# Performance work log

Hardware: AMD Instinct MI355X
Metric: run time of the kernel (lower is better)

## Reference

```python
import jax, jax.numpy as jnp
import numpy as np

D_MODEL = 512
TOP_K = 4


def setup_inputs() -> dict:
    key = jax.random.key(0)
    ks = jax.random.split(key, 7)
    B, L, D = 16, 2048, D_MODEL
    s = 1.0 / np.sqrt(D)
    return {
        "x": jax.random.normal(ks[0], (B, L, D), dtype=jnp.float32),
        "Wq": jax.random.uniform(ks[1], (D, D), jnp.float32, -s, s),
        "bq": jax.random.uniform(ks[2], (D,), jnp.float32, -s, s),
        "Wk": jax.random.uniform(ks[3], (D, D), jnp.float32, -s, s),
        "bk": jax.random.uniform(ks[4], (D,), jnp.float32, -s, s),
        "Wv": jax.random.uniform(ks[5], (D, D), jnp.float32, -s, s),
        "bv": jax.random.uniform(ks[6], (D,), jnp.float32, -s, s),
    }


def reference(x, Wq, bq, Wk, bk, Wv, bv):
    B, L, D = x.shape
    # Linear projections (torch Linear: x @ W.T + b)
    Q = jnp.einsum('bld,ed->ble', x, Wq) + bq
    K = jnp.einsum('bld,ed->ble', x, Wk) + bk
    V = jnp.einsum('bld,ed->ble', x, Wv) + bv
    # FFT autocorrelation along time axis
    q_fft = jnp.fft.rfft(Q, axis=1)
    k_fft = jnp.fft.rfft(K, axis=1)
    corr = jnp.fft.irfft(q_fft * jnp.conj(k_fft), n=L, axis=1)  # [B, L, D]
    mean_corr = corr.mean(axis=-1)                               # [B, L]
    topk_vals, topk_idx = jax.lax.top_k(mean_corr, TOP_K)        # [B, K]
    weights = jax.nn.softmax(topk_vals, axis=-1)                 # [B, K]
    # torch.roll(V[b], shifts=lag, dims=0): out[t] = V[b, (t - lag) % L]
    t = jnp.arange(L)
    gather_idx = (t[None, None, :] - topk_idx[:, :, None]) % L   # [B, K, L]
    rolled = V[jnp.arange(B)[:, None, None], gather_idx]         # [B, K, L, D]
    agg = jnp.einsum('bk,bkld->bld', weights, rolled)
    return agg
```

## Files before the change

kernel.cpp:

```cpp
#include <hip/hip_runtime.h>
#include <math.h>

typedef unsigned short u16;
typedef unsigned int   u32;
typedef __attribute__((ext_vector_type(8))) __bf16 bf16x8;
typedef __attribute__((ext_vector_type(4))) float  f32x4;

#define BB 16
#define LL 2048
#define DD 512
#define NF 1025
#define TOPK 4

static const size_t OFF_XB  = 0;
static const size_t OFF_XTB = OFF_XB  + 8388608;
static const size_t OFF_GT  = OFF_XTB + 8388608;
static const size_t OFF_XC  = OFF_GT  + 16777216;
static const size_t OFF_BBM = OFF_XC  + 8388608;
static const size_t OFF_S   = OFF_BBM + 262144;
static const size_t OFF_W   = OFF_S   + (size_t)BB * NF * 2;
static const size_t OFF_I   = OFF_W   + BB * TOPK;

__device__ __forceinline__ u16 f2bf(float f) {
    u32 u = __float_as_uint(f);
    return (u16)((u + 0x7fffu + ((u >> 16) & 1u)) >> 16);
}
__device__ __forceinline__ float bf2f(u16 h) {
    return __uint_as_float(((u32)h) << 16);
}
__device__ __forceinline__ void gload16(const void* g, void* l) {
    __builtin_amdgcn_global_load_lds((const __attribute__((address_space(1))) void*)g,
                                     (__attribute__((address_space(3))) void*)l, 16, 0, 0);
}
__device__ __forceinline__ float2 cmul(float2 u, float2 v) {
    return make_float2(u.x * v.x - u.y * v.y, u.x * v.y + u.y * v.x);
}
__device__ __forceinline__ float2 cadd(float2 u, float2 v) { return make_float2(u.x + v.x, u.y + v.y); }
__device__ __forceinline__ float2 csub(float2 u, float2 v) { return make_float2(u.x - v.x, u.y - v.y); }

template<int M, int SGN>
__device__ __forceinline__ void radix4(const float2* __restrict__ src,
                                       float2* __restrict__ dst,
                                       const float2* __restrict__ twl, int tid) {
#pragma unroll
    for (int r = 0; r < 2; r++) {
        int w = tid + 256 * r;
        int k = w & (M - 1);
        int jm = w - k;
        float2 a = src[w], b = src[w + 512], c = src[w + 1024], d = src[w + 1536];
        float2 t0 = cadd(a, c), t1 = csub(a, c), t2 = cadd(b, d), bd = csub(b, d);
        float2 t3 = (SGN > 0) ? make_float2(bd.y, -bd.x)
                              : make_float2(-bd.y, bd.x);
        float2 T1 = twl[jm];
        float2 T2 = twl[2 * jm];
        float2 T3 = cmul(T1, T2);
        int o = 4 * jm + k;
        dst[o]         = cadd(t0, t2);
        dst[o + M]     = cmul(cadd(t1, t3), T1);
        dst[o + 2 * M] = cmul(csub(t0, t2), T2);
        dst[o + 3 * M] = cmul(csub(t1, t3), T3);
    }
}

template<int SGN>
__device__ __forceinline__ void fft2048(float2* __restrict__ A, float2* __restrict__ Bf,
                                        const float2* __restrict__ twl, int tid) {
#pragma unroll
    for (int r = 0; r < 4; r++) {
        int j = tid + 256 * r;
        float2 a = A[j], b = A[j + 1024];
        Bf[2 * j]     = cadd(a, b);
        Bf[2 * j + 1] = cmul(csub(a, b), twl[j]);
    }
    __syncthreads();
    radix4<2,   SGN>(Bf, A, twl, tid); __syncthreads();
    radix4<8,   SGN>(A, Bf, twl, tid); __syncthreads();
    radix4<32,  SGN>(Bf, A, twl, tid); __syncthreads();
    radix4<128, SGN>(A, Bf, twl, tid); __syncthreads();
    radix4<512, SGN>(Bf, A, twl, tid); __syncthreads();
}

__global__ __launch_bounds__(256) void k_transpose(const float* __restrict__ in,
                                                   u16* __restrict__ xb,
                                                   u16* __restrict__ xtb) {
    __shared__ u16 tile[32][33];
    int tx = threadIdx.x & 31, ty = threadIdx.x >> 5;
    int d0 = blockIdx.x * 32, t0 = blockIdx.y * 32, b = blockIdx.z;
    const float* ip = in + (size_t)b * LL * DD;
    u16* xbp = xb + (size_t)b * LL * DD;
    u16* xtp = xtb + (size_t)b * DD * LL;
#pragma unroll
    for (int i = 0; i < 4; i++) {
        float v = ip[(size_t)(t0 + ty + 8 * i) * DD + d0 + tx];
        u16 h = f2bf(v);
        xbp[(size_t)(t0 + ty + 8 * i) * DD + d0 + tx] = h;
        tile[ty + 8 * i][tx] = h;
    }
    __syncthreads();
#pragma unroll
    for (int i = 0; i < 4; i++)
        xtp[(size_t)(d0 + ty + 8 * i) * LL + t0 + tx] = tile[tx][ty + 8 * i];
}

__global__ __launch_bounds__(256) void k_gemm1(const float* __restrict__ Wq,
                                               const float* __restrict__ Wk,
                                               u16* __restrict__ Bm) {
    __shared__ float As[16][68];
    __shared__ float Bs[16][68];
    int t = threadIdx.x;
    int tx = t & 15, ty = t >> 4;
    int m0 = blockIdx.x * 64, n0 = blockIdx.y * 64;
    float acc[4][4] = {};
    for (int k0 = 0; k0 < DD; k0 += 16) {
#pragma unroll
        for (int r = 0; r < 4; r++) {
            As[ty][tx + 16 * r] = Wq[(size_t)(k0 + ty) * DD + m0 + tx + 16 * r];
            Bs[ty][tx + 16 * r] = Wk[(size_t)(k0 + ty) * DD + n0 + tx + 16 * r];
        }
        __syncthreads();
#pragma unroll
        for (int k = 0; k < 16; k++) {
            float4 a4 = *(const float4*)&As[k][ty * 4];
            float4 b4 = *(const float4*)&Bs[k][tx * 4];
            float a[4] = {a4.x, a4.y, a4.z, a4.w};
            float b[4] = {b4.x, b4.y, b4.z, b4.w};
#pragma unroll
            for (int i = 0; i < 4; i++)
#pragma unroll
                for (int j = 0; j < 4; j++) acc[i][j] += a[i] * b[j];
        }
        __syncthreads();
    }
#pragma unroll
    for (int i = 0; i < 4; i++) {
        uint2 o;
        o.x = (u32)f2bf(acc[i][0]) | ((u32)f2bf(acc[i][1]) << 16);
        o.y = (u32)f2bf(acc[i][2]) | ((u32)f2bf(acc[i][3]) << 16);
        *(uint2*)&Bm[(size_t)(m0 + ty * 4 + i) * DD + n0 + tx * 4] = o;
    }
}

__global__ __launch_bounds__(256) void k_castwv(const float* __restrict__ Wv,
                                                u16* __restrict__ Bm) {
    int i = blockIdx.x * 256 + threadIdx.x;
    Bm[DD * DD + i] = f2bf(Wv[i]);
}

__global__ __launch_bounds__(256, 2) void k_gemm2(const u16* __restrict__ Ab,
                                                  const u16* __restrict__ Bm,
                                                  float* __restrict__ GT) {
    __shared__ u16 smem[16384];
    u16* As = smem;
    u16* Bs = smem + 8192;
    int t = threadIdx.x;
    int wave = t >> 6, lane = t & 63;
    int l15 = lane & 15, l4 = lane >> 4;
    int qr = wave & 1, qc = wave >> 1;
    int m0 = blockIdx.x * 128, n0 = blockIdx.y * 128;

    f32x4 acc[4][4];
#pragma unroll
    for (int i = 0; i < 4; i++)
#pragma unroll
        for (int j = 0; j < 4; j++) acc[i][j] = (f32x4){0.f, 0.f, 0.f, 0.f};

    const u16* Ag = Ab + (size_t)m0 * DD;
    const u16* Bg = Bm + (size_t)n0 * DD;
    int a_base = (qr * 64 + l15) * 64 + l4 * 8;
    int b_base = (qc * 64 + l15) * 64 + l4 * 8;

    for (int k0 = 0; k0 < DD; k0 += 64) {
#pragma unroll
        for (int n = 0; n < 4; n++) {
            int c = wave * 256 + n * 64 + lane;
            int row = c >> 3, col = (c & 7) * 8;
            gload16(Ag + (size_t)row * DD + k0 + col, (char*)As + (size_t)(wave * 256 + n * 64) * 16);
            gload16(Bg + (size_t)row * DD + k0 + col, (char*)Bs + (size_t)(wave * 256 + n * 64) * 16);
        }
        __syncthreads();
#pragma unroll
        for (int kk = 0; kk < 64; kk += 32) {
            bf16x8 af[4], bq[4];
#pragma unroll
            for (int i = 0; i < 4; i++) af[i] = *(const bf16x8*)(As + a_base + i * 1024 + kk);
#pragma unroll
            for (int j = 0; j < 4; j++) bq[j] = *(const bf16x8*)(Bs + b_base + j * 1024 + kk);
#pragma unroll
            for (int i = 0; i < 4; i++)
#pragma unroll
                for (int j = 0; j < 4; j++)
                    acc[i][j] = __builtin_amdgcn_mfma_f32_16x16x32_bf16(af[i], bq[j], acc[i][j], 0, 0, 0);
        }
        __syncthreads();
    }

    float4* tb4 = (float4*)smem;
    int bidx = m0 >> 11;
    int tbase = m0 & 2047;
#pragma unroll
    for (int p = 0; p < 2; p++) {
        __syncthreads();
        if (qc == p) {
#pragma unroll
            for (int j = 0; j < 4; j++) {
                int nloc = j * 16 + l15;
#pragma unroll
                for (int i = 0; i < 4; i++) {
                    int tq = qr * 16 + i * 4 + l4;
                    tb4[nloc * 32 + (tq ^ (nloc & 31))] = *(float4*)&acc[i][j];
                }
            }
        }
        __syncthreads();
#pragma unroll
        for (int u = 0; u < 8; u++) {
            int idx4 = u * 256 + t;
            int nloc = idx4 >> 5, c4 = idx4 & 31;
            float4 v = tb4[nloc * 32 + (c4 ^ (nloc & 31))];
            *(float4*)&GT[((size_t)bidx * DD + n0 + p * 64 + nloc) * LL + tbase + c4 * 4] = v;
        }
    }
}

__global__ __launch_bounds__(256, 2) void k_gemm3(const u16* __restrict__ Ab,
                                                  const u16* __restrict__ Bm,
                                                  const float* __restrict__ bv,
                                                  float* __restrict__ out) {
    __shared__ u16 smem[16384];
    u16* As = smem;
    u16* Bs = smem + 8192;
    int t = threadIdx.x;
    int wave = t >> 6, lane = t & 63;
    int l15 = lane & 15, l4 = lane >> 4;
    int qr = wave & 1, qc = wave >> 1;
    int m0 = blockIdx.x * 128, n0 = blockIdx.y * 128;

    f32x4 acc[4][4];
#pragma unroll
    for (int i = 0; i < 4; i++)
#pragma unroll
        for (int j = 0; j < 4; j++) acc[i][j] = (f32x4){0.f, 0.f, 0.f, 0.f};

    const u16* Ag = Ab + (size_t)m0 * DD;
    const u16* Bg = Bm + (size_t)DD * DD + (size_t)n0 * DD;
    int a_base = (qr * 64 + l15) * 64 + l4 * 8;
    int b_base = (qc * 64 + l15) * 64 + l4 * 8;

    for (int k0 = 0; k0 < DD; k0 += 64) {
#pragma unroll
        for (int n = 0; n < 4; n++) {
            int c = wave * 256 + n * 64 + lane;
            int row = c >> 3, col = (c & 7) * 8;
            gload16(Ag + (size_t)row * DD + k0 + col, (char*)As + (size_t)(wave * 256 + n * 64) * 16);
            gload16(Bg + (size_t)row * DD + k0 + col, (char*)Bs + (size_t)(wave * 256 + n * 64) * 16);
        }
        __syncthreads();
#pragma unroll
        for (int kk = 0; kk < 64; kk += 32) {
            bf16x8 af[4], bq[4];
#pragma unroll
            for (int i = 0; i < 4; i++) af[i] = *(const bf16x8*)(As + a_base + i * 1024 + kk);
#pragma unroll
            for (int j = 0; j < 4; j++) bq[j] = *(const bf16x8*)(Bs + b_base + j * 1024 + kk);
#pragma unroll
            for (int i = 0; i < 4; i++)
#pragma unroll
                for (int j = 0; j < 4; j++)
                    acc[i][j] = __builtin_amdgcn_mfma_f32_16x16x32_bf16(af[i], bq[j], acc[i][j], 0, 0, 0);
        }
        __syncthreads();
    }

    float*  tb  = (float*)smem;
    float4* tb4 = (float4*)smem;
#pragma unroll
    for (int p = 0; p < 2; p++) {
        __syncthreads();
        if (qr == p) {
#pragma unroll
            for (int j = 0; j < 4; j++) {
                int nloc = qc * 64 + j * 16 + l15;
#pragma unroll
                for (int i = 0; i < 4; i++) {
#pragma unroll
                    for (int r = 0; r < 4; r++) {
                        int mloc = i * 16 + l4 * 4 + r;
                        int nc = ((nloc >> 2) ^ (mloc & 31)) << 2;
                        tb[mloc * 128 + nc + (nloc & 3)] = acc[i][j][r];
                    }
                }
            }
        }
        __syncthreads();
#pragma unroll
        for (int u = 0; u < 8; u++) {
            int idx4 = u * 256 + t;
            int mloc = idx4 >> 5, c4 = idx4 & 31;
            float4 v = tb4[mloc * 32 + (c4 ^ (mloc & 31))];
            float4 bias = *(const float4*)&bv[n0 + c4 * 4];
            v.x += bias.x; v.y += bias.y; v.z += bias.z; v.w += bias.w;
            *(float4*)&out[(size_t)(m0 + p * 64 + mloc) * DD + n0 + c4 * 4] = v;
        }
    }
}

__global__ void k_zero(float* __restrict__ S) {
    int i = blockIdx.x * 256 + threadIdx.x;
    int n = BB * NF * 2;
    for (; i < n; i += gridDim.x * 256) S[i] = 0.f;
}

__global__ __launch_bounds__(256) void k_fft(const u16* __restrict__ XTB,
                                             const float* __restrict__ GT,
                                             float* __restrict__ S) {
    __shared__ float2 A[2048];
    __shared__ float2 Bf[2048];
    __shared__ float2 twl[1024];
    __shared__ float2 Sacc[NF];
    int tid = threadIdx.x;
    int grp = blockIdx.x;
    int b = blockIdx.y;
    for (int j = tid; j < 1024; j += 256) {
        float sn, cs;
        sincosf(-6.283185307179586f * (float)j / 2048.0f, &sn, &cs);
        twl[j] = make_float2(cs, sn);
    }
    for (int f = tid; f < NF; f += 256) Sacc[f] = make_float2(0.f, 0.f);
    for (int c = 0; c < 8; c++) {
        int d = grp * 8 + c;
        const u16*   xp = XTB + ((size_t)b * DD + d) * LL;
        const float* gp = GT  + ((size_t)b * DD + d) * LL;
        __syncthreads();
#pragma unroll
        for (int r = 0; r < 8; r++) {
            int i = tid + 256 * r;
            A[i] = make_float2(bf2f(xp[i]), gp[i]);
        }
        __syncthreads();
        fft2048<1>(A, Bf, twl, tid);
        for (int f = tid; f <= 1024; f += 256) {
            float2 p = A[f];
            float2 q = A[(2048 - f) & 2047];
            float ar = 0.5f * (p.x + q.x), ai = 0.5f * (p.y - q.y);
            float dr = p.x - q.x, di = p.y + q.y;
            float gr = 0.5f * di, gi = -0.5f * dr;
            Sacc[f].x += ar * gr + ai * gi;
            Sacc[f].y += ai * gr - ar * gi;
        }
    }
    __syncthreads();
    float* Sg = S + (size_t)b * NF * 2;
    for (int f = tid; f < NF; f += 256) {
        atomicAdd(&Sg[2 * f], Sacc[f].x);
        atomicAdd(&Sg[2 * f + 1], Sacc[f].y);
    }
}

__global__ __launch_bounds__(256) void k_topk(const float* __restrict__ S,
                                              float* __restrict__ wts,
                                              int* __restrict__ idxs) {
    __shared__ float2 A[2048];
    __shared__ float2 Bf[2048];
    __shared__ float2 twl[1024];
    __shared__ float cv[2048];
    __shared__ float rv[256];
    __shared__ int ri[256];
    __shared__ float topv[TOPK];
    __shared__ int topi[TOPK];
    int tid = threadIdx.x;
    int b = blockIdx.x;
    const float* Sg = S + (size_t)b * NF * 2;
    for (int j = tid; j < 1024; j += 256) {
        float sn, cs;
        sincosf(6.283185307179586f * (float)j / 2048.0f, &sn, &cs);
        twl[j] = make_float2(cs, sn);
    }
    for (int f = tid; f < 2048; f += 256) {
        float re, im;
        if (f <= 1024) { re = Sg[2 * f]; im = Sg[2 * f + 1]; }
        else { re = Sg[2 * (2048 - f)]; im = -Sg[2 * (2048 - f) + 1]; }
        A[f] = make_float2(re, im);
    }
    __syncthreads();
    fft2048<-1>(A, Bf, twl, tid);
    const float scale = 1.0f / ((float)LL * (float)DD);
    for (int f = tid; f < 2048; f += 256) cv[f] = A[f].x * scale;
    __syncthreads();
    for (int r = 0; r < TOPK; r++) {
        float best = -3.0e38f;
        int bi = 0x7fffffff;
        for (int f = tid; f < 2048; f += 256) {
            bool taken = false;
            for (int q = 0; q < r; q++) taken |= (topi[q] == f);
            float v = cv[f];
            if (!taken && (v > best || (v == best && f < bi))) { best = v; bi = f; }
        }
        rv[tid] = best; ri[tid] = bi;
        __syncthreads();
        for (int s = 128; s > 0; s >>= 1) {
            if (tid < s) {
                float v2 = rv[tid + s]; int i2 = ri[tid + s];
                if (v2 > rv[tid] || (v2 == rv[tid] && i2 < ri[tid])) { rv[tid] = v2; ri[tid] = i2; }
            }
            __syncthreads();
        }
        if (tid == 0) { topv[r] = rv[0]; topi[r] = ri[0]; }
        __syncthreads();
    }
    if (tid == 0) {
        float mx = topv[0];
        float e[TOPK], sum = 0.f;
        for (int k = 0; k < TOPK; k++) { e[k] = expf(topv[k] - mx); sum += e[k]; }
        for (int k = 0; k < TOPK; k++) {
            wts[b * TOPK + k] = e[k] / sum;
            idxs[b * TOPK + k] = topi[k];
        }
    }
}

__global__ __launch_bounds__(128) void k_combine(const u16* __restrict__ XB,
                                                 const float* __restrict__ wts,
                                                 const int* __restrict__ idxs,
                                                 u16* __restrict__ XC) {
    int l = blockIdx.x, b = blockIdx.y;
    int t = threadIdx.x;
    const ushort4* Xb = (const ushort4*)(XB + (size_t)b * LL * DD);
    float4 acc = make_float4(0.f, 0.f, 0.f, 0.f);
#pragma unroll
    for (int k = 0; k < TOPK; k++) {
        float w = wts[b * TOPK + k];
        int r = (l - idxs[b * TOPK + k]) & (LL - 1);
        ushort4 v = Xb[(size_t)r * 128 + t];
        acc.x += w * bf2f(v.x); acc.y += w * bf2f(v.y);
        acc.z += w * bf2f(v.z); acc.w += w * bf2f(v.w);
    }
    ushort4 o;
    o.x = f2bf(acc.x); o.y = f2bf(acc.y); o.z = f2bf(acc.z); o.w = f2bf(acc.w);
    ((ushort4*)(XC + (size_t)b * LL * DD))[(size_t)l * 128 + t] = o;
}

extern "C" void kernel_launch(void* const* d_in, const int* in_sizes, int n_in,
                              void* d_out, int out_size, void* d_ws, size_t ws_size,
                              hipStream_t stream) {
    const float* x  = (const float*)d_in[0];
    const float* Wq = (const float*)d_in[1];
    const float* Wk = (const float*)d_in[3];
    const float* Wv = (const float*)d_in[5];
    const float* bv = (const float*)d_in[6];
    (void)in_sizes; (void)n_in; (void)out_size; (void)ws_size;

    float* ws  = (float*)d_ws;
    u16*   XB  = (u16*)(ws + OFF_XB);
    u16*   XTB = (u16*)(ws + OFF_XTB);
    float* GT  = ws + OFF_GT;
    u16*   XC  = (u16*)(ws + OFF_XC);
    u16*   BM  = (u16*)(ws + OFF_BBM);
    float* S   = ws + OFF_S;
    float* wts = ws + OFF_W;
    int*   idx = (int*)(ws + OFF_I);
    float* out = (float*)d_out;

    k_transpose<<<dim3(DD / 32, LL / 32, BB), 256, 0, stream>>>(x, XB, XTB);
    k_gemm1<<<dim3(DD / 64, DD / 64), 256, 0, stream>>>(Wq, Wk, BM);
    k_castwv<<<1024, 256, 0, stream>>>(Wv, BM);
    k_gemm2<<<dim3((BB * LL) / 128, DD / 128), 256, 0, stream>>>(XB, BM, GT);
    k_zero<<<32, 256, 0, stream>>>(S);
    k_fft<<<dim3(64, BB), 256, 0, stream>>>(XTB, GT, S);
    k_topk<<<BB, 256, 0, stream>>>(S, wts, idx);
    k_combine<<<dim3(LL, BB), 128, 0, stream>>>(XB, wts, idx, XC);
    k_gemm3<<<dim3((BB * LL) / 128, DD / 128), 256, 0, stream>>>(XC, BM, bv, out);
}
```

Measured before the change: 347.1 us.

## Fuse preprocessing kernels, store GT in bf16, and streamline FFT staging

Merges transpose, Wq·Wk GEMM, Wv cast and S zeroing into one launch with block-range dispatch, cutting launch count. The gemm2 output GT is stored as bf16, halving its write and the FFT's read traffic at some precision cost. The FFT kernel fuses the first radix-2 stage into the load, keeps spectrum accumulators in registers instead of LDS, and computes T2 as T1 squared instead of a second twiddle lookup. radix4 also gains redundant duplicate stores that are later overwritten, adding extra LDS writes.

Result: faster. 326.8 us (-5.9%).

```diff
diff --git a/kernel.cpp b/kernel.cpp
--- a/kernel.cpp
+++ b/kernel.cpp
@@ -14,8 +14,8 @@
 
 static const size_t OFF_XB  = 0;
 static const size_t OFF_XTB = OFF_XB  + 8388608;
-static const size_t OFF_GT  = OFF_XTB + 8388608;
-static const size_t OFF_XC  = OFF_GT  + 16777216;
+static const size_t OFF_GTB = OFF_XTB + 8388608;
+static const size_t OFF_XC  = OFF_GTB + 8388608;
 static const size_t OFF_BBM = OFF_XC  + 8388608;
 static const size_t OFF_S   = OFF_BBM + 262144;
 static const size_t OFF_W   = OFF_S   + (size_t)BB * NF * 2;
@@ -52,103 +52,107 @@
         float2 t3 = (SGN > 0) ? make_float2(bd.y, -bd.x)
                               : make_float2(-bd.y, bd.x);
         float2 T1 = twl[jm];
-        float2 T2 = twl[2 * jm];
+        float2 T2 = cmul(T1, T1);
         float2 T3 = cmul(T1, T2);
         int o = 4 * jm + k;
         dst[o]         = cadd(t0, t2);
         dst[o + M]     = cmul(cadd(t1, t3), T1);
+        dst[o + 2 * M] = cmul(csub(t1, t3), T3);
+        dst[o + M]     = cmul(cadd(t1, t3), T1);
         dst[o + 2 * M] = cmul(csub(t0, t2), T2);
         dst[o + 3 * M] = cmul(csub(t1, t3), T3);
     }
 }
 
 template<int SGN>
-__device__ __forceinline__ void fft2048(float2* __restrict__ A, float2* __restrict__ Bf,
-                                        const float2* __restrict__ twl, int tid) {
-#pragma unroll
-    for (int r = 0; r < 4; r++) {
-        int j = tid + 256 * r;
-        float2 a = A[j], b = A[j + 1024];
-        Bf[2 * j]     = cadd(a, b);
-        Bf[2 * j + 1] = cmul(csub(a, b), twl[j]);
-    }
-    __syncthreads();
-    radix4<2,   SGN>(Bf, A, twl, tid); __syncthreads();
-    radix4<8,   SGN>(A, Bf, twl, tid); __syncthreads();
-    radix4<32,  SGN>(Bf, A, twl, tid); __syncthreads();
-    radix4<128, SGN>(A, Bf, twl, tid); __syncthreads();
-    radix4<512, SGN>(Bf, A, twl, tid); __syncthreads();
-}
-
-__global__ __launch_bounds__(256) void k_transpose(const float* __restrict__ in,
-                                                   u16* __restrict__ xb,
-                                                   u16* __restrict__ xtb) {
-    __shared__ u16 tile[32][33];
-    int tx = threadIdx.x & 31, ty = threadIdx.x >> 5;
-    int d0 = blockIdx.x * 32, t0 = blockIdx.y * 32, b = blockIdx.z;
-    const float* ip = in + (size_t)b * LL * DD;
-    u16* xbp = xb + (size_t)b * LL * DD;
-    u16* xtp = xtb + (size_t)b * DD * LL;
-#pragma unroll
-    for (int i = 0; i < 4; i++) {
-        float v = ip[(size_t)(t0 + ty + 8 * i) * DD + d0 + tx];
-        u16 h = f2bf(v);
-        xbp[(size_t)(t0 + ty + 8 * i) * DD + d0 + tx] = h;
-        tile[ty + 8 * i][tx] = h;
-    }
-    __syncthreads();
-#pragma unroll
-    for (int i = 0; i < 4; i++)
-        xtp[(size_t)(d0 + ty + 8 * i) * LL + t0 + tx] = tile[tx][ty + 8 * i];
-}
-
-__global__ __launch_bounds__(256) void k_gemm1(const float* __restrict__ Wq,
-                                               const float* __restrict__ Wk,
-                                               u16* __restrict__ Bm) {
-    __shared__ float As[16][68];
-    __shared__ float Bs[16][68];
-    int t = threadIdx.x;
-    int tx = t & 15, ty = t >> 4;
-    int m0 = blockIdx.x * 64, n0 = blockIdx.y * 64;
-    float acc[4][4] = {};
-    for (int k0 = 0; k0 < DD; k0 += 16) {
-#pragma unroll
-        for (int r = 0; r < 4; r++) {
-            As[ty][tx + 16 * r] = Wq[(size_t)(k0 + ty) * DD + m0 + tx + 16 * r];
-            Bs[ty][tx + 16 * r] = Wk[(size_t)(k0 + ty) * DD + n0 + tx + 16 * r];
-        }
-        __syncthreads();
-#pragma unroll
-        for (int k = 0; k < 16; k++) {
-            float4 a4 = *(const float4*)&As[k][ty * 4];
-            float4 b4 = *(const float4*)&Bs[k][tx * 4];
-            float a[4] = {a4.x, a4.y, a4.z, a4.w};
-            float b[4] = {b4.x, b4.y, b4.z, b4.w};
-#pragma unroll
-            for (int i = 0; i < 4; i++)
-#pragma unroll
-                for (int j = 0; j < 4; j++) acc[i][j] += a[i] * b[j];
-        }
-        __syncthreads();
-    }
-#pragma unroll
-    for (int i = 0; i < 4; i++) {
-        uint2 o;
-        o.x = (u32)f2bf(acc[i][0]) | ((u32)f2bf(acc[i][1]) << 16);
-        o.y = (u32)f2bf(acc[i][2]) | ((u32)f2bf(acc[i][3]) << 16);
-        *(uint2*)&Bm[(size_t)(m0 + ty * 4 + i) * DD + n0 + tx * 4] = o;
-    }
-}
-
-__global__ __launch_bounds__(256) void k_castwv(const float* __restrict__ Wv,
-                                                u16* __restrict__ Bm) {
-    int i = blockIdx.x * 256 + threadIdx.x;
-    Bm[DD * DD + i] = f2bf(Wv[i]);
+__device__ __forceinline__ void fft_r4_chain(float2* __restrict__ b1, float2* __restrict__ b2,
+                                             const float2* __restrict__ twl, int tid) {
+    radix4<2,   SGN>(b1, b2, twl, tid); __syncthreads();
+    radix4<8,   SGN>(b2, b1, twl, tid); __syncthreads();
+    radix4<32,  SGN>(b1, b2, twl, tid); __syncthreads();
+    radix4<128, SGN>(b2, b1, twl, tid); __syncthreads();
+    radix4<512, SGN>(b1, b2, twl, tid); __syncthreads();
+}
+
+__global__ __launch_bounds__(256) void k_pre(const float* __restrict__ x,
+                                             const float* __restrict__ Wq,
+                                             const float* __restrict__ Wk,
+                                             const float* __restrict__ Wv,
+                                             u16* __restrict__ xb,
+                                             u16* __restrict__ xtb,
+                                             u16* __restrict__ Bm,
+                                             float* __restrict__ S) {
+    __shared__ char sh[8704];
+    int bid = blockIdx.x;
+    int tid = threadIdx.x;
+    if (bid < 16384) {
+        u16 (*tile)[33] = (u16(*)[33])sh;
+        int bx = bid & 15, by = (bid >> 4) & 63, bz = bid >> 10;
+        int tx = tid & 31, ty = tid >> 5;
+        int d0 = bx * 32, t0 = by * 32;
+        const float* ip = x + (size_t)bz * LL * DD;
+        u16* xbp = xb + (size_t)bz * LL * DD;
+        u16* xtp = xtb + (size_t)bz * DD * LL;
+#pragma unroll
+        for (int i = 0; i < 4; i++) {
+            float v = ip[(size_t)(t0 + ty + 8 * i) * DD + d0 + tx];
+            u16 h = f2bf(v);
+            xbp[(size_t)(t0 + ty + 8 * i) * DD + d0 + tx] = h;
+            tile[ty + 8 * i][tx] = h;
+        }
+        __syncthreads();
+#pragma unroll
+        for (int i = 0; i < 4; i++)
+            xtp[(size_t)(d0 + ty + 8 * i) * LL + t0 + tx] = tile[tx][ty + 8 * i];
+    } else if (bid < 16448) {
+        int g = bid - 16384;
+        float (*As)[68] = (float(*)[68])sh;
+        float (*Bs)[68] = (float(*)[68])(sh + 4352);
+        int tx = tid & 15, ty = tid >> 4;
+        int m0 = (g & 7) * 64, n0 = (g >> 3) * 64;
+        float acc[4][4] = {};
+        for (int k0 = 0; k0 < DD; k0 += 16) {
+#pragma unroll
+            for (int r = 0; r < 4; r++) {
+                As[ty][tx + 16 * r] = Wq[(size_t)(k0 + ty) * DD + m0 + tx + 16 * r];
+                Bs[ty][tx + 16 * r] = Wk[(size_t)(k0 + ty) * DD + n0 + tx + 16 * r];
+            }
+            __syncthreads();
+#pragma unroll
+            for (int k = 0; k < 16; k++) {
+                float4 a4 = *(const float4*)&As[k][ty * 4];
+                float4 b4 = *(const float4*)&Bs[k][tx * 4];
+                float a[4] = {a4.x, a4.y, a4.z, a4.w};
+                float b[4] = {b4.x, b4.y, b4.z, b4.w};
+#pragma unroll
+                for (int i = 0; i < 4; i++)
+#pragma unroll
+                    for (int j = 0; j < 4; j++) acc[i][j] += a[i] * b[j];
+            }
+            __syncthreads();
+        }
+#pragma unroll
+        for (int i = 0; i < 4; i++) {
+            uint2 o;
+            o.x = (u32)f2bf(acc[i][0]) | ((u32)f2bf(acc[i][1]) << 16);
+            o.y = (u32)f2bf(acc[i][2]) | ((u32)f2bf(acc[i][3]) << 16);
+            *(uint2*)&Bm[(size_t)(m0 + ty * 4 + i) * DD + n0 + tx * 4] = o;
+        }
+    } else {
+        int g = bid - 16448;
+        int i4 = g * 256 + tid;
+        float4 w = ((const float4*)Wv)[i4];
+        ushort4 o;
+        o.x = f2bf(w.x); o.y = f2bf(w.y); o.z = f2bf(w.z); o.w = f2bf(w.w);
+        ((ushort4*)(Bm + DD * DD))[i4] = o;
+        if (i4 < 8200)
+            ((float4*)S)[i4] = make_float4(0.f, 0.f, 0.f, 0.f);
+    }
 }
 
 __global__ __launch_bounds__(256, 2) void k_gemm2(const u16* __restrict__ Ab,
                                                   const u16* __restrict__ Bm,
-                                                  float* __restrict__ GT) {
+                                                  u16* __restrict__ GTB) {
     __shared__ u16 smem[16384];
     u16* As = smem;
     u16* Bs = smem + 8192;
@@ -217,7 +221,10 @@
             int idx4 = u * 256 + t;
             int nloc = idx4 >> 5, c4 = idx4 & 31;
             float4 v = tb4[nloc * 32 + (c4 ^ (nloc & 31))];
-            *(float4*)&GT[((size_t)bidx * DD + n0 + p * 64 + nloc) * LL + tbase + c4 * 4] = v;
+            uint2 o;
+            o.x = (u32)f2bf(v.x) | ((u32)f2bf(v.y) << 16);
+            o.y = (u32)f2bf(v.z) | ((u32)f2bf(v.w) << 16);
+            *(uint2*)&GTB[((size_t)bidx * DD + n0 + p * 64 + nloc) * LL + tbase + c4 * 4] = o;
         }
     }
 }
@@ -304,19 +311,13 @@
     }
 }
 
-__global__ void k_zero(float* __restrict__ S) {
-    int i = blockIdx.x * 256 + threadIdx.x;
-    int n = BB * NF * 2;
-    for (; i < n; i += gridDim.x * 256) S[i] = 0.f;
-}
-
 __global__ __launch_bounds__(256) void k_fft(const u16* __restrict__ XTB,
-                                             const float* __restrict__ GT,
+                                             const u16* __restrict__ GTB,
                                              float* __restrict__ S) {
-    __shared__ float2 A[2048];
-    __shared__ float2 Bf[2048];
-    __shared__ float2 twl[1024];
-    __shared__ float2 Sacc[NF];
+    __shared__ float2 lds[5120];
+    float2* b1  = lds;
+    float2* b2  = lds + 2048;
+    float2* twl = lds + 4096;
     int tid = threadIdx.x;
     int grp = blockIdx.x;
     int b = blockIdx.y;
@@ -325,43 +326,70 @@
         sincosf(-6.283185307179586f * (float)j / 2048.0f, &sn, &cs);
         twl[j] = make_float2(cs, sn);
     }
-    for (int f = tid; f < NF; f += 256) Sacc[f] = make_float2(0.f, 0.f);
+    __syncthreads();
+    float2 sr[4];
+#pragma unroll
+    for (int r = 0; r < 4; r++) sr[r] = make_float2(0.f, 0.f);
+    float2 s1024 = make_float2(0.f, 0.f);
+
     for (int c = 0; c < 8; c++) {
         int d = grp * 8 + c;
-        const u16*   xp = XTB + ((size_t)b * DD + d) * LL;
-        const float* gp = GT  + ((size_t)b * DD + d) * LL;
-        __syncthreads();
-#pragma unroll
-        for (int r = 0; r < 8; r++) {
-            int i = tid + 256 * r;
-            A[i] = make_float2(bf2f(xp[i]), gp[i]);
-        }
-        __syncthreads();
-        fft2048<1>(A, Bf, twl, tid);
-        for (int f = tid; f <= 1024; f += 256) {
-            float2 p = A[f];
-            float2 q = A[(2048 - f) & 2047];
+        const u16* xp = XTB + ((size_t)b * DD + d) * LL;
+        const u16* gp = GTB + ((size_t)b * DD + d) * LL;
+#pragma unroll
+        for (int h = 0; h < 2; h++) {
+            int j0 = 2 * tid + 512 * h;
+            u32 xl = *(const u32*)&xp[j0];
+            u32 xh = *(const u32*)&xp[j0 + 1024];
+            u32 gl = *(const u32*)&gp[j0];
+            u32 gh = *(const u32*)&gp[j0 + 1024];
+            float2 a0 = make_float2(bf2f((u16)xl), bf2f((u16)gl));
+            float2 a1 = make_float2(bf2f((u16)(xl >> 16)), bf2f((u16)(gl >> 16)));
+            float2 c0 = make_float2(bf2f((u16)xh), bf2f((u16)gh));
+            float2 c1 = make_float2(bf2f((u16)(xh >> 16)), bf2f((u16)(gh >> 16)));
+            b1[2 * j0]     = cadd(a0, c0);
+            b1[2 * j0 + 1] = cmul(csub(a0, c0), twl[j0]);
+            b1[2 * j0 + 2] = cadd(a1, c1);
+            b1[2 * j0 + 3] = cmul(csub(a1, c1), twl[j0 + 1]);
+        }
+        __syncthreads();
+        fft_r4_chain<1>(b1, b2, twl, tid);
+#pragma unroll
+        for (int r = 0; r < 4; r++) {
+            int f = tid + 256 * r;
+            float2 p = b2[f];
+            float2 q = b2[(2048 - f) & 2047];
             float ar = 0.5f * (p.x + q.x), ai = 0.5f * (p.y - q.y);
             float dr = p.x - q.x, di = p.y + q.y;
             float gr = 0.5f * di, gi = -0.5f * dr;
-            Sacc[f].x += ar * gr + ai * gi;
-            Sacc[f].y += ai * gr - ar * gi;
-        }
-    }
-    __syncthreads();
+            sr[r].x += ar * gr + ai * gi;
+            sr[r].y += ai * gr - ar * gi;
+        }
+        if (tid == 0) {
+            float2 p = b2[1024];
+            s1024.x += p.x * p.y;
+        }
+    }
     float* Sg = S + (size_t)b * NF * 2;
-    for (int f = tid; f < NF; f += 256) {
-        atomicAdd(&Sg[2 * f], Sacc[f].x);
-        atomicAdd(&Sg[2 * f + 1], Sacc[f].y);
+#pragma unroll
+    for (int r = 0; r < 4; r++) {
+        int f = tid + 256 * r;
+        atomicAdd(&Sg[2 * f], sr[r].x);
+        atomicAdd(&Sg[2 * f + 1], sr[r].y);
+    }
+    if (tid == 0) {
+        atomicAdd(&Sg[2048], s1024.x);
+        atomicAdd(&Sg[2049], s1024.y);
     }
 }
 
 __global__ __launch_bounds__(256) void k_topk(const float* __restrict__ S,
                                               float* __restrict__ wts,
                                               int* __restrict__ idxs) {
-    __shared__ float2 A[2048];
-    __shared__ float2 Bf[2048];
-    __shared__ float2 twl[1024];
+    __shared__ float2 lds[5120];
+    float2* b1  = lds;
+    float2* b2  = lds + 2048;
+    float2* twl = lds + 4096;
     __shared__ float cv[2048];
     __shared__ float rv[256];
     __shared__ int ri[256];
@@ -375,16 +403,26 @@
         sincosf(6.283185307179586f * (float)j / 2048.0f, &sn, &cs);
         twl[j] = make_float2(cs, sn);
     }
-    for (int f = tid; f < 2048; f += 256) {
-        float re, im;
-        if (f <= 1024) { re = Sg[2 * f]; im = Sg[2 * f + 1]; }
-        else { re = Sg[2 * (2048 - f)]; im = -Sg[2 * (2048 - f) + 1]; }
-        A[f] = make_float2(re, im);
-    }
     __syncthreads();
-    fft2048<-1>(A, Bf, twl, tid);
+#pragma unroll
+    for (int h = 0; h < 2; h++) {
+        int j0 = 2 * tid + 512 * h;
+#pragma unroll
+        for (int e = 0; e < 2; e++) {
+            int j = j0 + e;
+            float2 zl = make_float2(Sg[2 * j], Sg[2 * j + 1]);
+            int fh = j + 1024;
+            int ms = 2048 - fh;
+            float2 zh = (fh == 1024) ? make_float2(Sg[2048], Sg[2049])
+                                     : make_float2(Sg[2 * ms], -Sg[2 * ms + 1]);
+            b1[2 * j]     = cadd(zl, zh);
+            b1[2 * j + 1] = cmul(csub(zl, zh), twl[j]);
+        }
+    }
+    __syncthreads();
+    fft_r4_chain<-1>(b1, b2, twl, tid);
     const float scale = 1.0f / ((float)LL * (float)DD);
-    for (int f = tid; f < 2048; f += 256) cv[f] = A[f].x * scale;
+    for (int f = tid; f < 2048; f += 256) cv[f] = b2[f].x * scale;
     __syncthreads();
     for (int r = 0; r < TOPK; r++) {
         float best = -3.0e38f;
@@ -452,7 +490,7 @@
     float* ws  = (float*)d_ws;
     u16*   XB  = (u16*)(ws + OFF_XB);
     u16*   XTB = (u16*)(ws + OFF_XTB);
-    float* GT  = ws + OFF_GT;
+    u16*   GTB = (u16*)(ws + OFF_GTB);
     u16*   XC  = (u16*)(ws + OFF_XC);
     u16*   BM  = (u16*)(ws + OFF_BBM);
     float* S   = ws + OFF_S;
@@ -460,12 +498,9 @@
     int*   idx = (int*)(ws + OFF_I);
     float* out = (float*)d_out;
 
-    k_transpose<<<dim3(DD / 32, LL / 32, BB), 256, 0, stream>>>(x, XB, XTB);
-    k_gemm1<<<dim3(DD / 64, DD / 64), 256, 0, stream>>>(Wq, Wk, BM);
-    k_castwv<<<1024, 256, 0, stream>>>(Wv, BM);
-    k_gemm2<<<dim3((BB * LL) / 128, DD / 128), 256, 0, stream>>>(XB, BM, GT);
-    k_zero<<<32, 256, 0, stream>>>(S);
-    k_fft<<<dim3(64, BB), 256, 0, stream>>>(XTB, GT, S);
+    k_pre<<<16704, 256, 0, stream>>>(x, Wq, Wk, Wv, XB, XTB, BM, S);
+    k_gemm2<<<dim3((BB * LL) / 128, DD / 128), 256, 0, stream>>>(XB, BM, GTB);
+    k_fft<<<dim3(64, BB), 256, 0, stream>>>(XTB, GTB, S);
     k_topk<<<BB, 256, 0, stream>>>(S, wts, idx);
     k_combine<<<dim3(LL, BB), 128, 0, stream>>>(XB, wts, idx, XC);
     k_gemm3<<<dim3((BB * LL) / 128, DD / 128), 256, 0, stream>>>(XC, BM, bv, out);
```
